# Kernel optimization log

Measured on AMD Instinct MI355X. Metric: run time of the kernel, lower is better.

The kernel has to match this reference:

```python
import jax, jax.numpy as jnp
import numpy as np

N_EXPERTS = 8
Z_DIM = 128
HID = 1024
OUT = 3072  # e.g. 3x32x32 flattened generator output
BATCH = 2048


def hash_vectors(z, n):
    """Deterministic per-sample hash -> expert index in [0, n).

    Proxy for the repo's hash_vectors (which hashes the latent vector):
    quantize |z|, sum over feature dim, mod n. Non-differentiable by design.
    """
    return jnp.mod(jnp.floor(jnp.abs(z) * 1000.0).sum(axis=1).astype(jnp.int32), n)


def setup_inputs() -> dict:
    key = jax.random.key(0)
    kz, k1, kb1, k2, kb2 = jax.random.split(key, 5)
    z = jax.random.normal(kz, (BATCH, Z_DIM), dtype=jnp.float32)
    s1 = 1.0 / np.sqrt(Z_DIM)
    s2 = 1.0 / np.sqrt(HID)
    # Stacked per-expert MLP params (each expert independently initialized,
    # mirroring reset_parameters on each deepcopy).
    W1 = jax.random.uniform(k1, (N_EXPERTS, Z_DIM, HID), jnp.float32, -s1, s1)
    b1 = jax.random.uniform(kb1, (N_EXPERTS, HID), jnp.float32, -s1, s1)
    W2 = jax.random.uniform(k2, (N_EXPERTS, HID, OUT), jnp.float32, -s2, s2)
    b2 = jax.random.uniform(kb2, (N_EXPERTS, OUT), jnp.float32, -s2, s2)
    return {"z": z, "W1": W1, "b1": b1, "W2": W2, "b2": b2}


def reference(z, W1, b1, W2, b2):
    # Hard routing: each sample i goes to expert idx[i].
    idx = hash_vectors(z, N_EXPERTS)  # [B]
    # Dense compute-all-experts then select (vectorized replacement for the
    # per-sample Python loop in the original forward).
    h = jax.nn.relu(jnp.einsum('bi,eih->beh', z, W1) + b1[None, :, :])  # [B,E,H]
    y = jnp.einsum('beh,eho->beo', h, W2) + b2[None, :, :]              # [B,E,O]
    out = jnp.take_along_axis(y, idx[:, None, None], axis=1)[:, 0, :]   # [B,O]
    return out
```

## Files before the change

kernel.cpp:

```cpp
#include <hip/hip_runtime.h>
#include <hip/hip_bf16.h>


#define BATCH 2048
#define ZD 128
#define HID 1024
#define OUTD 3072
#define NEXP 8
#define MAXTF 24

typedef short bf16x8 __attribute__((ext_vector_type(8)));
typedef float f32x4 __attribute__((ext_vector_type(4)));


__global__ __launch_bounds__(256) void route_kernel(const float* __restrict__ z,
                                                    __hip_bfloat16* __restrict__ zb,
                                                    int* counts, int* bucket) {
    __shared__ int lcnt[NEXP];
    __shared__ int gbase[NEXP];
    int t = threadIdx.x;
    if (t < NEXP) lcnt[t] = 0;
    __syncthreads();

    int s = blockIdx.x * 32 + (t >> 3);
    int li = t & 7;
    const float* zp = z + (size_t)s * ZD + li * 16;
    float sum = 0.f;
    union { bf16x8 v8; __hip_bfloat16 h[8]; } u0, u1;
#pragma unroll
    for (int i = 0; i < 4; i++) {
        float4 v = ((const float4*)zp)[i];
        sum += floorf(fabsf(v.x) * 1000.0f) + floorf(fabsf(v.y) * 1000.0f) +
               floorf(fabsf(v.z) * 1000.0f) + floorf(fabsf(v.w) * 1000.0f);
        __hip_bfloat16* dst = (i < 2) ? &u0.h[i * 4] : &u1.h[(i - 2) * 4];
        dst[0] = __float2bfloat16(v.x);
        dst[1] = __float2bfloat16(v.y);
        dst[2] = __float2bfloat16(v.z);
        dst[3] = __float2bfloat16(v.w);
    }
    bf16x8* zo = (bf16x8*)(zb + (size_t)s * ZD + li * 16);
    zo[0] = u0.v8;
    zo[1] = u1.v8;

    sum += __shfl_down(sum, 4);
    sum += __shfl_down(sum, 2);
    sum += __shfl_down(sum, 1);
    int e = 0, lpos = 0;
    if (li == 0) {
        e = ((int)sum) & 7;
        lpos = atomicAdd(&lcnt[e], 1);
    }
    __syncthreads();
    if (t < NEXP) gbase[t] = atomicAdd(&counts[t], lcnt[t]);
    __syncthreads();
    if (li == 0) bucket[e * BATCH + gbase[e] + lpos] = s;
}

__global__ void scan_kernel(const int* __restrict__ counts, int* ntl,
                            int* texp, int* perm, const int* __restrict__ bucket) {
    __shared__ int soff[NEXP + 1];
    __shared__ int scnt[NEXP];
    if (threadIdx.x == 0) {
        int o = 0;
        for (int e = 0; e < NEXP; e++) {
            scnt[e] = counts[e];
            soff[e] = o;
            o += (scnt[e] + 127) & ~127;
        }
        soff[NEXP] = o;
        *ntl = o / 128;
    }
    __syncthreads();
    int total = soff[NEXP];
    for (int r = threadIdx.x; r < total; r += blockDim.x) {
        int e = 0;
        while (r >= soff[e + 1]) e++;
        int i = r - soff[e];
        perm[r] = (i < scnt[e]) ? bucket[e * BATCH + i] : -1;
        if ((r & 127) == 0) texp[r / 128] = e;
    }
}

__global__ __launch_bounds__(256, 4) void gemm1_fast(
    const __hip_bfloat16* __restrict__ zb, const float* __restrict__ W1,
    const float* __restrict__ b1, const int* __restrict__ ntl,
    const int* __restrict__ texp, const int* __restrict__ perm,
    __hip_bfloat16* __restrict__ H) {
    int mt = blockIdx.y;
    if (mt >= 2 * (*ntl)) return;
    int e = texp[mt >> 1];
    int n0 = blockIdx.x * 64;

    __shared__ __align__(16) __hip_bfloat16 As[2][64 * 64];
    __shared__ __align__(16) __hip_bfloat16 Bs[2][64 * 64];

    int tid = threadIdx.x;
    int lane = tid & 63, wave = tid >> 6;
    int cc = lane & 15, q = lane >> 4;
    int mw = (wave >> 1) * 32, nw = (wave & 1) * 32;

    int sc = tid & 7, rg = tid >> 3;
    int r0 = perm[mt * 64 + rg];      if (r0 < 0) r0 = 0;
    int r1 = perm[mt * 64 + rg + 32]; if (r1 < 0) r1 = 0;
    const __hip_bfloat16* Ap0 = zb + (size_t)r0 * ZD + sc * 8;
    const __hip_bfloat16* Ap1 = zb + (size_t)r1 * ZD + sc * 8;
    int awb = rg * 64 + (sc ^ (rg & 7)) * 8;

    int bkc = tid & 7, bn2 = (tid >> 3) * 2;
    const float* Bgf = W1 + (size_t)e * ZD * HID + (size_t)(bkc * 8) * HID + n0 + bn2;
    int bwb[2];
#pragma unroll
    for (int j = 0; j < 2; j++)
        bwb[j] = ((bn2 + j) * 8 + (bkc ^ ((bn2 + j) & 7))) * 8;

    int A0 = (mw + cc) * 64, B0 = (nw + cc) * 64;
    int X0 = (q ^ (cc & 7)) * 8, X1 = ((4 + q) ^ (cc & 7)) * 8;

    float bias[2];
#pragma unroll
    for (int j = 0; j < 2; j++) bias[j] = b1[(size_t)e * HID + n0 + nw + j * 16 + cc];

    f32x4 zero4 = {0.f, 0.f, 0.f, 0.f};
    f32x4 acc[2][2];
#pragma unroll
    for (int i = 0; i < 2; i++)
#pragma unroll
        for (int j = 0; j < 2; j++) acc[i][j] = zero4;

    bf16x8 ga0 = *(const bf16x8*)Ap0;
    bf16x8 ga1 = *(const bf16x8*)Ap1;
    float2 braw[8];
#pragma unroll
    for (int i = 0; i < 8; i++) braw[i] = *(const float2*)(Bgf + (size_t)i * HID);

#pragma unroll
    for (int it = 0; it < 2; ++it) {
        __hip_bfloat16* Ac = As[it];
        __hip_bfloat16* Bc = Bs[it];
        union { bf16x8 v8; __hip_bfloat16 h[8]; } gbv[2];
#pragma unroll
        for (int i = 0; i < 8; i++) {
            gbv[0].h[i] = __float2bfloat16(braw[i].x);
            gbv[1].h[i] = __float2bfloat16(braw[i].y);
        }
        *(bf16x8*)(Ac + awb) = ga0;
        *(bf16x8*)(Ac + awb + 2048) = ga1;
#pragma unroll
        for (int j = 0; j < 2; j++) *(bf16x8*)(Bc + bwb[j]) = gbv[j].v8;
        if (it == 0) {
            ga0 = *(const bf16x8*)(Ap0 + 64);
            ga1 = *(const bf16x8*)(Ap1 + 64);
#pragma unroll
            for (int i = 0; i < 8; i++)
                braw[i] = *(const float2*)(Bgf + (size_t)(64 + i) * HID);
        }
        __syncthreads();
#pragma unroll
        for (int kh = 0; kh < 2; ++kh) {
            int X = kh ? X1 : X0;
            bf16x8 af[2], bfr[2];
#pragma unroll
            for (int i = 0; i < 2; i++) af[i] = *(const bf16x8*)(Ac + A0 + i * 1024 + X);
#pragma unroll
            for (int j = 0; j < 2; j++) bfr[j] = *(const bf16x8*)(Bc + B0 + j * 1024 + X);
#pragma unroll
            for (int i = 0; i < 2; i++)
#pragma unroll
                for (int j = 0; j < 2; j++)
                    acc[i][j] = __builtin_amdgcn_mfma_f32_16x16x32_bf16(af[i], bfr[j],
                                                                        acc[i][j], 0, 0, 0);
        }
    }
#pragma unroll
    for (int i = 0; i < 2; i++)
#pragma unroll
        for (int r = 0; r < 4; r++) {
            int m = mw + i * 16 + q * 4 + r;
            __hip_bfloat16* hp = H + (size_t)(mt * 64 + m) * HID + n0 + nw + cc;
#pragma unroll
            for (int j = 0; j < 2; j++)
                hp[j * 16] = __float2bfloat16(fmaxf(acc[i][j][r] + bias[j], 0.f));
        }
}

__global__ __launch_bounds__(256, 2) void gemm2_fast(
    const __hip_bfloat16* __restrict__ H, const float* __restrict__ W2,
    const float* __restrict__ b2, const int* __restrict__ ntl,
    const int* __restrict__ texp, const int* __restrict__ perm,
    float* __restrict__ out) {
    int mt = blockIdx.y;
    if (mt >= *ntl) return;
    int e = texp[mt];
    int n0 = blockIdx.x * 128;

    __shared__ __align__(16) __hip_bfloat16 As[2][128 * 64];
    __shared__ __align__(16) __hip_bfloat16 Bs[2][128 * 64];
    __shared__ int rows_s[128];

    int tid = threadIdx.x;
    if (tid < 128) rows_s[tid] = perm[mt * 128 + tid];

    int lane = tid & 63, wave = tid >> 6;
    int cc = lane & 15, q = lane >> 4;
    int mw = (wave >> 1) * 64, nw = (wave & 1) * 64;

    int sr = tid >> 3, sc = tid & 7;
    int awbase = sr * 64 + (sc ^ (sr & 7)) * 8;
    const __hip_bfloat16* Ag = H + ((size_t)mt * 128 + sr) * HID + sc * 8;
    int bkc = tid & 7, bn = (tid >> 3) * 4;
    const float* Bgf = W2 + (size_t)e * HID * OUTD + (size_t)(bkc * 8) * OUTD + n0 + bn;
    int bwb[4];
#pragma unroll
    for (int j = 0; j < 4; j++)
        bwb[j] = (bn + j) * 64 + ((bkc ^ ((bn + j) & 7))) * 8;

    int A0 = (mw + cc) * 64, B0 = (nw + cc) * 64;
    int X0 = (q ^ (cc & 7)) * 8, X1 = ((4 + q) ^ (cc & 7)) * 8;

    float bias[4];
#pragma unroll
    for (int j = 0; j < 4; j++) bias[j] = b2[(size_t)e * OUTD + n0 + nw + j * 16 + cc];

    f32x4 zero4 = {0.f, 0.f, 0.f, 0.f};
    f32x4 acc[4][4];
#pragma unroll
    for (int i = 0; i < 4; i++)
#pragma unroll
        for (int j = 0; j < 4; j++) acc[i][j] = zero4;

    bf16x8 ga[4];
    float4 braw[8];
#pragma unroll
    for (int p = 0; p < 4; p++) ga[p] = *(const bf16x8*)(Ag + (size_t)p * 32 * HID);
#pragma unroll
    for (int i = 0; i < 8; i++) braw[i] = *(const float4*)(Bgf + (size_t)i * OUTD);

    const int NIT = HID / 64;
    for (int it = 0; it < NIT; ++it) {
        __hip_bfloat16* Ac = As[it & 1];
        __hip_bfloat16* Bc = Bs[it & 1];
        union { bf16x8 v8; __hip_bfloat16 h[8]; } gb[4];
#pragma unroll
        for (int i = 0; i < 8; i++) {
            gb[0].h[i] = __float2bfloat16(braw[i].x);
            gb[1].h[i] = __float2bfloat16(braw[i].y);
            gb[2].h[i] = __float2bfloat16(braw[i].z);
            gb[3].h[i] = __float2bfloat16(braw[i].w);
        }
#pragma unroll
        for (int p = 0; p < 4; p++) *(bf16x8*)(Ac + awbase + p * 2048) = ga[p];
#pragma unroll
        for (int j = 0; j < 4; j++) *(bf16x8*)(Bc + bwb[j]) = gb[j].v8;
        if (it + 1 < NIT) {
            int k1 = (it + 1) * 64;
#pragma unroll
            for (int p = 0; p < 4; p++)
                ga[p] = *(const bf16x8*)(Ag + (size_t)p * 32 * HID + k1);
#pragma unroll
            for (int i = 0; i < 8; i++)
                braw[i] = *(const float4*)(Bgf + (size_t)(k1 + i) * OUTD);
        }
        __syncthreads();
#pragma unroll
        for (int kh = 0; kh < 2; ++kh) {
            int X = kh ? X1 : X0;
            bf16x8 af[4], bfr[4];
#pragma unroll
            for (int i = 0; i < 4; i++) af[i] = *(const bf16x8*)(Ac + A0 + i * 1024 + X);
#pragma unroll
            for (int j = 0; j < 4; j++) bfr[j] = *(const bf16x8*)(Bc + B0 + j * 1024 + X);
#pragma unroll
            for (int i = 0; i < 4; i++)
#pragma unroll
                for (int j = 0; j < 4; j++)
                    acc[i][j] = __builtin_amdgcn_mfma_f32_16x16x32_bf16(af[i], bfr[j],
                                                                        acc[i][j], 0, 0, 0);
        }
    }
#pragma unroll
    for (int i = 0; i < 4; i++)
#pragma unroll
        for (int r = 0; r < 4; r++) {
            int m = mw + i * 16 + q * 4 + r;
            int orow = rows_s[m];
            if (orow >= 0) {
                float* op = out + (size_t)orow * OUTD + n0 + nw + cc;
#pragma unroll
                for (int j = 0; j < 4; j++) op[j * 16] = acc[i][j][r] + bias[j];
            }
        }
}

extern "C" void kernel_launch(void* const* d_in, const int* in_sizes, int n_in,
                              void* d_out, int out_size, void* d_ws, size_t ws_size,
                              hipStream_t stream) {
    const float* z  = (const float*)d_in[0];
    const float* W1 = (const float*)d_in[1];
    const float* b1 = (const float*)d_in[2];
    const float* W2 = (const float*)d_in[3];
    const float* b2 = (const float*)d_in[4];
    float* out = (float*)d_out;

    char* ws = (char*)d_ws;
    int* counts = (int*)ws;
    int* ntl    = (int*)(ws + 64);
    int* texp   = (int*)(ws + 128);
    int* perm   = (int*)(ws + 256);
    int* bucket = (int*)(ws + 12544);
    __hip_bfloat16* zb  = (__hip_bfloat16*)(ws + 78080);
    __hip_bfloat16* Hb  = (__hip_bfloat16*)(ws + 602368);

    hipMemsetAsync(counts, 0, 64, stream);
    hipLaunchKernelGGL(route_kernel, dim3(BATCH / 32), dim3(256), 0, stream,
                       z, zb, counts, bucket);
    hipLaunchKernelGGL(scan_kernel, dim3(1), dim3(256), 0, stream,
                       counts, ntl, texp, perm, bucket);
    hipLaunchKernelGGL(gemm1_fast, dim3(HID / 64, 2 * MAXTF), dim3(256), 0, stream,
                       zb, W1, b1, ntl, texp, perm, Hb);
    hipLaunchKernelGGL(gemm2_fast, dim3(OUTD / 128, MAXTF), dim3(256), 0, stream,
                       Hb, W2, b2, ntl, texp, perm, out);
}
```

Before: 200.9 us.

## Simplify routing into single-block scatter and halve gemm2 N tile

Routing now writes a per-sample expert id, and a single-block scan kernel counts, pads and scatters sample indices into perm with shared-memory atomics. This removes the global count atomics, the bucket buffer and the memset. The gemm2 tile is cut from 128 to 64 output columns, which doubles the grid and lowers register and LDS use, with occupancy raised to 3 blocks. In exchange, each W2 and H element is reused less per block, and the scatter order inside each expert becomes nondeterministic.

```diff
diff --git a/kernel.cpp b/kernel.cpp
--- a/kernel.cpp
+++ b/kernel.cpp
@@ -15,13 +15,8 @@
 
 __global__ __launch_bounds__(256) void route_kernel(const float* __restrict__ z,
                                                     __hip_bfloat16* __restrict__ zb,
-                                                    int* counts, int* bucket) {
-    __shared__ int lcnt[NEXP];
-    __shared__ int gbase[NEXP];
+                                                    int* __restrict__ eid) {
     int t = threadIdx.x;
-    if (t < NEXP) lcnt[t] = 0;
-    __syncthreads();
-
     int s = blockIdx.x * 32 + (t >> 3);
     int li = t & 7;
     const float* zp = z + (size_t)s * ZD + li * 16;
@@ -45,39 +40,44 @@
     sum += __shfl_down(sum, 4);
     sum += __shfl_down(sum, 2);
     sum += __shfl_down(sum, 1);
-    int e = 0, lpos = 0;
-    if (li == 0) {
-        e = ((int)sum) & 7;
-        lpos = atomicAdd(&lcnt[e], 1);
-    }
+    if (li == 0) eid[s] = ((int)sum) & 7;
+}
+
+__global__ __launch_bounds__(256) void scan_kernel(const int* __restrict__ eid,
+                                                   int* ntl, int* texp, int* perm) {
+    __shared__ int cnt[NEXP];
+    __shared__ int soff[NEXP + 1];
+    __shared__ int cur[NEXP];
+    int t = threadIdx.x;
+    if (t < NEXP) cnt[t] = 0;
     __syncthreads();
-    if (t < NEXP) gbase[t] = atomicAdd(&counts[t], lcnt[t]);
+    for (int s = t; s < BATCH; s += 256) atomicAdd(&cnt[eid[s]], 1);
     __syncthreads();
-    if (li == 0) bucket[e * BATCH + gbase[e] + lpos] = s;
-}
-
-__global__ void scan_kernel(const int* __restrict__ counts, int* ntl,
-                            int* texp, int* perm, const int* __restrict__ bucket) {
-    __shared__ int soff[NEXP + 1];
-    __shared__ int scnt[NEXP];
-    if (threadIdx.x == 0) {
+    if (t == 0) {
         int o = 0;
         for (int e = 0; e < NEXP; e++) {
-            scnt[e] = counts[e];
             soff[e] = o;
-            o += (scnt[e] + 127) & ~127;
+            cur[e] = o;
+            o += (cnt[e] + 127) & ~127;
         }
         soff[NEXP] = o;
         *ntl = o / 128;
     }
     __syncthreads();
     int total = soff[NEXP];
-    for (int r = threadIdx.x; r < total; r += blockDim.x) {
-        int e = 0;
-        while (r >= soff[e + 1]) e++;
-        int i = r - soff[e];
-        perm[r] = (i < scnt[e]) ? bucket[e * BATCH + i] : -1;
-        if ((r & 127) == 0) texp[r / 128] = e;
+    for (int r = t; r < total; r += 256) {
+        perm[r] = -1;
+        if ((r & 127) == 0) {
+            int e = 0;
+            while (r >= soff[e + 1]) e++;
+            texp[r / 128] = e;
+        }
+    }
+    __syncthreads();
+    for (int s = t; s < BATCH; s += 256) {
+        int e = eid[s];
+        int pos = atomicAdd(&cur[e], 1);
+        perm[pos] = s;
     }
 }
 
@@ -183,7 +183,7 @@
         }
 }
 
-__global__ __launch_bounds__(256, 2) void gemm2_fast(
+__global__ __launch_bounds__(256, 3) void gemm2_fast(
     const __hip_bfloat16* __restrict__ H, const float* __restrict__ W2,
     const float* __restrict__ b2, const int* __restrict__ ntl,
     const int* __restrict__ texp, const int* __restrict__ perm,
@@ -191,10 +191,10 @@
     int mt = blockIdx.y;
     if (mt >= *ntl) return;
     int e = texp[mt];
-    int n0 = blockIdx.x * 128;
+    int n0 = blockIdx.x * 64;
 
     __shared__ __align__(16) __hip_bfloat16 As[2][128 * 64];
-    __shared__ __align__(16) __hip_bfloat16 Bs[2][128 * 64];
+    __shared__ __align__(16) __hip_bfloat16 Bs[2][64 * 64];
     __shared__ int rows_s[128];
 
     int tid = threadIdx.x;
@@ -202,55 +202,53 @@
 
     int lane = tid & 63, wave = tid >> 6;
     int cc = lane & 15, q = lane >> 4;
-    int mw = (wave >> 1) * 64, nw = (wave & 1) * 64;
+    int mw = (wave >> 1) * 64, nw = (wave & 1) * 32;
 
     int sr = tid >> 3, sc = tid & 7;
     int awbase = sr * 64 + (sc ^ (sr & 7)) * 8;
     const __hip_bfloat16* Ag = H + ((size_t)mt * 128 + sr) * HID + sc * 8;
-    int bkc = tid & 7, bn = (tid >> 3) * 4;
+    int bkc = tid & 7, bn = (tid >> 3) * 2;
     const float* Bgf = W2 + (size_t)e * HID * OUTD + (size_t)(bkc * 8) * OUTD + n0 + bn;
-    int bwb[4];
-#pragma unroll
-    for (int j = 0; j < 4; j++)
-        bwb[j] = (bn + j) * 64 + ((bkc ^ ((bn + j) & 7))) * 8;
+    int bwb[2];
+#pragma unroll
+    for (int j = 0; j < 2; j++)
+        bwb[j] = ((bn + j) * 8 + (bkc ^ ((bn + j) & 7))) * 8;
 
     int A0 = (mw + cc) * 64, B0 = (nw + cc) * 64;
     int X0 = (q ^ (cc & 7)) * 8, X1 = ((4 + q) ^ (cc & 7)) * 8;
 
-    float bias[4];
-#pragma unroll
-    for (int j = 0; j < 4; j++) bias[j] = b2[(size_t)e * OUTD + n0 + nw + j * 16 + cc];
+    float bias[2];
+#pragma unroll
+    for (int j = 0; j < 2; j++) bias[j] = b2[(size_t)e * OUTD + n0 + nw + j * 16 + cc];
 
     f32x4 zero4 = {0.f, 0.f, 0.f, 0.f};
-    f32x4 acc[4][4];
+    f32x4 acc[4][2];
 #pragma unroll
     for (int i = 0; i < 4; i++)
 #pragma unroll
-        for (int j = 0; j < 4; j++) acc[i][j] = zero4;
+        for (int j = 0; j < 2; j++) acc[i][j] = zero4;
 
     bf16x8 ga[4];
-    float4 braw[8];
+    float2 braw[8];
 #pragma unroll
     for (int p = 0; p < 4; p++) ga[p] = *(const bf16x8*)(Ag + (size_t)p * 32 * HID);
 #pragma unroll
-    for (int i = 0; i < 8; i++) braw[i] = *(const float4*)(Bgf + (size_t)i * OUTD);
+    for (int i = 0; i < 8; i++) braw[i] = *(const float2*)(Bgf + (size_t)i * OUTD);
 
     const int NIT = HID / 64;
     for (int it = 0; it < NIT; ++it) {
         __hip_bfloat16* Ac = As[it & 1];
         __hip_bfloat16* Bc = Bs[it & 1];
-        union { bf16x8 v8; __hip_bfloat16 h[8]; } gb[4];
+        union { bf16x8 v8; __hip_bfloat16 h[8]; } gb[2];
 #pragma unroll
         for (int i = 0; i < 8; i++) {
             gb[0].h[i] = __float2bfloat16(braw[i].x);
             gb[1].h[i] = __float2bfloat16(braw[i].y);
-            gb[2].h[i] = __float2bfloat16(braw[i].z);
-            gb[3].h[i] = __float2bfloat16(braw[i].w);
         }
 #pragma unroll
         for (int p = 0; p < 4; p++) *(bf16x8*)(Ac + awbase + p * 2048) = ga[p];
 #pragma unroll
-        for (int j = 0; j < 4; j++) *(bf16x8*)(Bc + bwb[j]) = gb[j].v8;
+        for (int j = 0; j < 2; j++) *(bf16x8*)(Bc + bwb[j]) = gb[j].v8;
         if (it + 1 < NIT) {
             int k1 = (it + 1) * 64;
 #pragma unroll
@@ -258,21 +256,21 @@
                 ga[p] = *(const bf16x8*)(Ag + (size_t)p * 32 * HID + k1);
 #pragma unroll
             for (int i = 0; i < 8; i++)
-                braw[i] = *(const float4*)(Bgf + (size_t)(k1 + i) * OUTD);
+                braw[i] = *(const float2*)(Bgf + (size_t)(k1 + i) * OUTD);
         }
         __syncthreads();
 #pragma unroll
         for (int kh = 0; kh < 2; ++kh) {
             int X = kh ? X1 : X0;
-            bf16x8 af[4], bfr[4];
+            bf16x8 af[4], bfr[2];
 #pragma unroll
             for (int i = 0; i < 4; i++) af[i] = *(const bf16x8*)(Ac + A0 + i * 1024 + X);
 #pragma unroll
-            for (int j = 0; j < 4; j++) bfr[j] = *(const bf16x8*)(Bc + B0 + j * 1024 + X);
+            for (int j = 0; j < 2; j++) bfr[j] = *(const bf16x8*)(Bc + B0 + j * 1024 + X);
 #pragma unroll
             for (int i = 0; i < 4; i++)
 #pragma unroll
-                for (int j = 0; j < 4; j++)
+                for (int j = 0; j < 2; j++)
                     acc[i][j] = __builtin_amdgcn_mfma_f32_16x16x32_bf16(af[i], bfr[j],
                                                                         acc[i][j], 0, 0, 0);
         }
@@ -286,7 +284,7 @@
             if (orow >= 0) {
                 float* op = out + (size_t)orow * OUTD + n0 + nw + cc;
 #pragma unroll
-                for (int j = 0; j < 4; j++) op[j * 16] = acc[i][j][r] + bias[j];
+                for (int j = 0; j < 2; j++) op[j * 16] = acc[i][j][r] + bias[j];
             }
         }
 }
@@ -302,21 +300,19 @@
     float* out = (float*)d_out;
 
     char* ws = (char*)d_ws;
-    int* counts = (int*)ws;
-    int* ntl    = (int*)(ws + 64);
-    int* texp   = (int*)(ws + 128);
-    int* perm   = (int*)(ws + 256);
-    int* bucket = (int*)(ws + 12544);
-    __hip_bfloat16* zb  = (__hip_bfloat16*)(ws + 78080);
-    __hip_bfloat16* Hb  = (__hip_bfloat16*)(ws + 602368);
-
-    hipMemsetAsync(counts, 0, 64, stream);
+    int* ntl  = (int*)ws;
+    int* texp = (int*)(ws + 64);
+    int* perm = (int*)(ws + 256);
+    int* eid  = (int*)(ws + 12544);
+    __hip_bfloat16* zb = (__hip_bfloat16*)(ws + 78080);
+    __hip_bfloat16* Hb = (__hip_bfloat16*)(ws + 602368);
+
     hipLaunchKernelGGL(route_kernel, dim3(BATCH / 32), dim3(256), 0, stream,
-                       z, zb, counts, bucket);
+                       z, zb, eid);
     hipLaunchKernelGGL(scan_kernel, dim3(1), dim3(256), 0, stream,
-                       counts, ntl, texp, perm, bucket);
+                       eid, ntl, texp, perm);
     hipLaunchKernelGGL(gemm1_fast, dim3(HID / 64, 2 * MAXTF), dim3(256), 0, stream,
                        zb, W1, b1, ntl, texp, perm, Hb);
-    hipLaunchKernelGGL(gemm2_fast, dim3(OUTD / 128, MAXTF), dim3(256), 0, stream,
+    hipLaunchKernelGGL(gemm2_fast, dim3(OUTD / 64, MAXTF), dim3(256), 0, stream,
                        Hb, W2, b2, ntl, texp, perm, out);
 }
```

Measured after the change: 227.6 us. 1.13x slower.
